# Optimization experiments

Hardware: AMD Instinct MI355X
Metric: run time of the kernel (lower is better)

Reference implementation:

```python
import jax, jax.numpy as jnp
import numpy as np

B, N, E = 2, 8192, 131072
IN_C, NF = 4, 32
F_IN = IN_C * NF          # 128, = in_channels * num_features
HID, H, OUT = 64, 8, 64   # hidden_features, nheads, out_features
NEG_SLOPE = 0.2           # GATv2Conv default negative_slope


def setup_inputs() -> dict:
    key = jax.random.key(0)
    ks = jax.random.split(key, 12)
    x = jax.random.normal(ks[0], (B, N, IN_C, NF), dtype=jnp.float32)
    edge_index = jax.random.randint(ks[1], (2, E), 0, N, dtype=jnp.int32)

    def w(k, shape, fan_in):
        return jax.random.normal(k, shape, dtype=jnp.float32) / np.sqrt(fan_in).astype(np.float32)

    # GATv2 layer 1: lin_l (source), lin_r (target), attention vector a, bias
    W1l = w(ks[2], (F_IN, H * HID), F_IN)
    W1r = w(ks[3], (F_IN, H * HID), F_IN)
    att1 = w(ks[4], (H, HID), HID)
    b1 = jnp.zeros((H * HID,), dtype=jnp.float32)
    # GATv2 layer 2: input channels = H*HID = 512
    W2l = w(ks[5], (H * HID, H * OUT), H * HID)
    W2r = w(ks[6], (H * HID, H * OUT), H * HID)
    att2 = w(ks[7], (H, OUT), OUT)
    b2 = jnp.zeros((H * OUT,), dtype=jnp.float32)
    return {"x": x, "edge_index": edge_index,
            "W1l": W1l, "W1r": W1r, "att1": att1, "b1": b1,
            "W2l": W2l, "W2r": W2r, "att2": att2, "b2": b2}


def _gatv2_layer(f, src, dst, Wl, Wr, att, b, heads, ch):
    # f: [N, F_in]; src/dst: [E'] (self-loops included)
    xl = (f @ Wl).reshape(N, heads, ch)   # source-side transform (messages)
    xr = (f @ Wr).reshape(N, heads, ch)   # target-side transform
    e = jax.nn.leaky_relu(xl[src] + xr[dst], NEG_SLOPE)     # [E', H, C]
    logits = jnp.einsum('ehc,hc->eh', e, att)               # [E', H]
    # softmax over incoming edges of each target node
    m = jax.lax.stop_gradient(jax.ops.segment_max(logits, dst, num_segments=N))
    a = jnp.exp(logits - m[dst])
    denom = jax.ops.segment_sum(a, dst, num_segments=N)     # [N, H] (>0: self-loops)
    a = a / denom[dst]
    out = jax.ops.segment_sum(xl[src] * a[:, :, None], dst, num_segments=N)
    return out.reshape(N, heads * ch) + b


def reference(x, edge_index, W1l, W1r, att1, b1, W2l, W2r, att2, b2):
    # add self-loops (PyG GATv2Conv default add_self_loops=True)
    loops = jnp.arange(N, dtype=edge_index.dtype)
    src = jnp.concatenate([edge_index[0], loops])
    dst = jnp.concatenate([edge_index[1], loops])
    feats = x.reshape(B, N, F_IN)  # view(batch, nodes, in_channels*num_features)

    def per_graph(f):
        h = _gatv2_layer(f, src, dst, W1l, W1r, att1, b1, H, HID)   # [N, 512]
        return _gatv2_layer(h, src, dst, W2l, W2r, att2, b2, H, OUT)  # [N, 512]

    h_prime = jax.vmap(per_graph)(feats)   # [B, N, H*OUT]
    return jax.nn.elu(h_prime)             # concat=True branch
```

## Files before the change

kernel.cpp:

```cpp
#include <hip/hip_runtime.h>
#include <cstdint>

#define NN 8192
#define NT 16384
#define EE 131072
#define EPAD (EE + NN)
#define SPAD (EPAD + 3 * NN)
#define FIN 128
#define CH 512
#define NH 8
#define NEG 0.2f

typedef __attribute__((ext_vector_type(8))) short short8;
typedef __attribute__((ext_vector_type(4))) unsigned short u16x4;
typedef __attribute__((ext_vector_type(4))) float f32x4;
typedef __attribute__((ext_vector_type(4))) int i32x4;

__device__ inline unsigned short bf16rne(float x) {
    unsigned u = __float_as_uint(x);
    unsigned r = (u + 0x7FFFu + ((u >> 16) & 1u)) >> 16;
    return (unsigned short)r;
}
__device__ inline float bf16tof(unsigned short h) {
    return __uint_as_float((unsigned)h << 16);
}
__device__ inline void gload16(const void* g, void* l) {
    __builtin_amdgcn_global_load_lds((const __attribute__((address_space(1))) void*)g,
                                     (__attribute__((address_space(3))) void*)l, 16, 0, 0);
}
template <int CTRL>
__device__ inline float dpp_add(float x) {
    int v = __builtin_amdgcn_update_dpp(0, __float_as_int(x), CTRL, 0xF, 0xF, true);
    return x + __int_as_float(v);
}


__global__ __launch_bounds__(256) void k_deg(const int* __restrict__ ei, int* __restrict__ deg) {
    int e = blockIdx.x * 256 + threadIdx.x;
    if (e >= EPAD) return;
    int dst = (e < EE) ? ei[EE + e] : (e - EE);
    atomicAdd(&deg[dst], 1);
}

__global__ __launch_bounds__(1024) void k_scan(const int* __restrict__ deg, int* __restrict__ rowptr) {
    __shared__ int wsum[16];
    int t = threadIdx.x;
    int lane = t & 63, wid = t >> 6;
    int loc[8];
    int s = 0;
#pragma unroll
    for (int i = 0; i < 8; i++) { loc[i] = s; s += (deg[t * 8 + i] + 3) & ~3; }
    int inc = s;
#pragma unroll
    for (int off = 1; off < 64; off <<= 1) {
        int v = __shfl_up(inc, off);
        if (lane >= off) inc += v;
    }
    if (lane == 63) wsum[wid] = inc;
    __syncthreads();
    if (wid == 0 && lane < 16) {
        int v = wsum[lane];
#pragma unroll
        for (int off = 1; off < 16; off <<= 1) {
            int u = __shfl_up(v, off);
            if (lane >= off) v += u;
        }
        wsum[lane] = v;
    }
    __syncthreads();
    int wbase = (wid == 0) ? 0 : wsum[wid - 1];
    int base = wbase + inc - s;
#pragma unroll
    for (int i = 0; i < 8; i++) rowptr[t * 8 + i] = base + loc[i];
    if (t == 1023) rowptr[NN] = wbase + inc;
}

__global__ __launch_bounds__(256) void k_scatter(const int* __restrict__ ei, const int* __restrict__ rowptr,
                                                 int* __restrict__ cursor, int* __restrict__ ssrc) {
    int e = blockIdx.x * 256 + threadIdx.x;
    if (e >= EPAD) return;
    int src = (e < EE) ? ei[e] : (e - EE);
    int dst = (e < EE) ? ei[EE + e] : (e - EE);
    int pos = rowptr[dst] + atomicAdd(&cursor[dst], 1);
    ssrc[pos] = src;
}

__global__ __launch_bounds__(256) void k_pad(const int* __restrict__ rowptr, const int* __restrict__ deg,
                                             int* __restrict__ ssrc) {
    int n = blockIdx.x * 256 + threadIdx.x;
    if (n >= NN) return;
    int e = rowptr[n] + deg[n], pe = rowptr[n + 1];
    for (int i = e; i < pe; i++) ssrc[i] = 0;
}


__global__ __launch_bounds__(256) void k_cvt_ah(const float* __restrict__ F,
                                                unsigned short* __restrict__ Ah, int n4) {
    int i = blockIdx.x * 256 + threadIdx.x;
    if (i >= n4) return;
    f32x4 v = ((const f32x4*)F)[i];
#pragma unroll
    for (int c = 0; c < 4; c++) Ah[i * 4 + c] = bf16rne(v[c]);
}

template <int K>
__global__ __launch_bounds__(256) void k_cvt_w(const float* __restrict__ Wl, const float* __restrict__ Wr,
                                               unsigned short* __restrict__ Wh) {
    int idx = blockIdx.x * 256 + threadIdx.x;
    int n = idx / K, k = idx % K;
    const float* W = (n < 512) ? Wl : Wr;
    Wh[idx] = bf16rne(W[k * 512 + (n & 511)]);
}


template <int K, int BK>
__global__ __launch_bounds__(256) void k_gemm_mfma(const unsigned short* __restrict__ Ah,
                                                   const unsigned short* __restrict__ Bh,
                                                   unsigned short* __restrict__ XLb,
                                                   float* __restrict__ XR) {
    const int NS = BK / 8;
    __shared__ unsigned short sAh[NS][128][8], sBh[NS][128][8];
    int tid = threadIdx.x;
    int l = tid & 63;
    int w = tid >> 6, wm = w >> 1, wn = w & 1;
    int m0 = blockIdx.x * 128, n0 = blockIdx.y * 128;
    int lr = l & 15, kh = l >> 4;
    f32x4 acc[4][4] = {};

    for (int k0 = 0; k0 < K; k0 += BK) {
#pragma unroll
        for (int g = 0; g < NS / 2; g++) {
            int cell = g * 256 + tid;
            int ckh = cell >> 7, cr = cell & 127;
            int ka = k0 + ckh * 8;
            gload16(Ah + (size_t)(m0 + cr) * K + ka, &sAh[ckh][cr][0]);
            gload16(Bh + (size_t)(n0 + cr) * K + ka, &sBh[ckh][cr][0]);
        }
        __syncthreads();
#pragma unroll
        for (int kk = 0; kk < BK / 32; kk++) {
            int ks = kk * 4 + kh;
            short8 fah[4], fbh[4];
#pragma unroll
            for (int i = 0; i < 4; i++) {
                fah[i] = *(const short8*)&sAh[ks][wm * 64 + i * 16 + lr][0];
                fbh[i] = *(const short8*)&sBh[ks][wn * 64 + i * 16 + lr][0];
            }
#pragma unroll
            for (int i = 0; i < 4; i++)
#pragma unroll
                for (int j = 0; j < 4; j++)
                    acc[i][j] = __builtin_amdgcn_mfma_f32_16x16x32_bf16(fah[i], fbh[j], acc[i][j], 0, 0, 0);
        }
        __syncthreads();
    }
    int colt = n0 + wn * 64;
    int cb = colt & 511;
    if (colt < 512) {
#pragma unroll
        for (int i = 0; i < 4; i++) {
            int mg = m0 + wm * 64 + i * 16 + kh * 4;
#pragma unroll
            for (int j = 0; j < 4; j++) {
                int cg = cb + j * 16 + lr;
#pragma unroll
                for (int q = 0; q < 4; q++)
                    XLb[(size_t)(mg + q) * CH + cg] = bf16rne(acc[i][j][q]);
            }
        }
    } else {
#pragma unroll
        for (int i = 0; i < 4; i++) {
            int mg = m0 + wm * 64 + i * 16 + kh * 4;
#pragma unroll
            for (int j = 0; j < 4; j++) {
                int cg = cb + j * 16 + lr;
#pragma unroll
                for (int q = 0; q < 4; q++)
                    XR[(size_t)(mg + q) * CH + cg] = acc[i][j][q];
            }
        }
    }
}


#define GATHER(CX, IV)                                                         \
  {                                                                            \
    CX[0] = *(const u16x4*)(XLg + (size_t)IV[0] * CH);                         \
    CX[1] = *(const u16x4*)(XLg + (size_t)IV[1] * CH);                         \
    CX[2] = *(const u16x4*)(XLg + (size_t)IV[2] * CH);                         \
    CX[3] = *(const u16x4*)(XLg + (size_t)IV[3] * CH);                         \
  }

#define PROCESS(CX, cb)                                                        \
  {                                                                            \
    float f[4][4];                                                             \
    _Pragma("unroll") for (int e = 0; e < 4; e++)                              \
      _Pragma("unroll") for (int r = 0; r < 4; r++)                            \
        f[e][r] = bf16tof(CX[e][r]);                                           \
    float z[4];                                                                \
    _Pragma("unroll") for (int e = 0; e < 4; e++) {                            \
      float s = 0.f;                                                           \
      _Pragma("unroll") for (int r = 0; r < 4; r++) {                          \
        float t = f[e][r] + xrv[r];                                            \
        t = fmaxf(t, NEG * t);                                                 \
        s += t * atv[r];                                                       \
      }                                                                        \
      z[e] = s;                                                                \
    }                                                                          \
    _Pragma("unroll") for (int e = 0; e < 4; e++) {                            \
      z[e] = dpp_add<0xB1>(z[e]);                                              \
      z[e] = dpp_add<0x4E>(z[e]);                                              \
      z[e] = dpp_add<0x124>(z[e]);                                             \
      z[e] = dpp_add<0x128>(z[e]);                                             \
    }                                                                          \
    _Pragma("unroll") for (int e = 1; e < 4; e++)                              \
      if ((cb) + e >= end) z[e] = -1e30f;                                      \
    float mc = fmaxf(fmaxf(z[0], z[1]), fmaxf(z[2], z[3]));                    \
    if (__ballot(mc > mh + 8.f) == 0ULL) {                                     \
      float p0 = __expf(z[0] - mh), p1 = __expf(z[1] - mh);                    \
      float p2 = __expf(z[2] - mh), p3 = __expf(z[3] - mh);                    \
      sh += (p0 + p1) + (p2 + p3);                                             \
      _Pragma("unroll") for (int r = 0; r < 4; r++)                            \
        acc[r] += p0 * f[0][r] + p1 * f[1][r] + p2 * f[2][r] + p3 * f[3][r];   \
    } else {                                                                   \
      float nm = fmaxf(mh, mc);                                                \
      float sc = __expf(mh - nm);                                              \
      float p0 = __expf(z[0] - nm), p1 = __expf(z[1] - nm);                    \
      float p2 = __expf(z[2] - nm), p3 = __expf(z[3] - nm);                    \
      sh = sh * sc + (p0 + p1) + (p2 + p3);                                    \
      mh = nm;                                                                 \
      _Pragma("unroll") for (int r = 0; r < 4; r++)                            \
        acc[r] = acc[r] * sc + p0 * f[0][r] + p1 * f[1][r] + p2 * f[2][r] +    \
                 p3 * f[3][r];                                                 \
    }                                                                          \
  }

template <int WRITE_BF16>
__global__ __launch_bounds__(256) void k_node5(const unsigned short* __restrict__ XLb,
                                               const float* __restrict__ XR,
                                               const int* __restrict__ rowptr,
                                               const int* __restrict__ deg,
                                               const int* __restrict__ ssrc,
                                               const float* __restrict__ att,
                                               const float* __restrict__ bias,
                                               float* __restrict__ OUT,
                                               unsigned short* __restrict__ OAh) {
    int w = threadIdx.x >> 6;
    int nid = blockIdx.x * 2 + (w >> 1);
    int g = w & 1;
    int l = threadIdx.x & 63;
    int node = nid & (NN - 1);
    int beg = rowptr[node], pend = rowptr[node + 1];
    int end = beg + deg[node];
    int hb = g * 256 + l * 4;

    const unsigned short* XLg = XLb + (size_t)(nid >> 13) * NN * CH + hb;
    f32x4 xrv = *(const f32x4*)(XR + (size_t)nid * CH + hb);
    f32x4 atv = *(const f32x4*)(att + hb);
    f32x4 acc = {0.f, 0.f, 0.f, 0.f};
    float mh = -1e30f, sh = 0.f;

    i32x4 iA = *(const i32x4*)(ssrc + beg);
    i32x4 iB = iA;
    u16x4 curA[4], curB[4];
    GATHER(curA, iA);
    if (beg + 4 < pend) iB = *(const i32x4*)(ssrc + beg + 4);

    int base = beg;
    while (true) {
        if (base + 4 < pend) GATHER(curB, iB);
        if (base + 8 < pend) iA = *(const i32x4*)(ssrc + base + 8);
        PROCESS(curA, base);
        base += 4;
        if (base >= pend) break;
        if (base + 4 < pend) GATHER(curA, iA);
        if (base + 8 < pend) iB = *(const i32x4*)(ssrc + base + 8);
        PROCESS(curB, base);
        base += 4;
        if (base >= pend) break;
    }

    float inv = 1.f / sh;
    f32x4 biasv = *(const f32x4*)(bias + hb);
    size_t ob = (size_t)nid * CH + hb;
    if (WRITE_BF16) {
        u16x4 hv;
#pragma unroll
        for (int r = 0; r < 4; r++) {
            float wv = acc[r] * inv + biasv[r];
            hv[r] = bf16rne(wv);
        }
        *(u16x4*)(OAh + ob) = hv;
    } else {
        f32x4 ov;
#pragma unroll
        for (int r = 0; r < 4; r++) {
            float wv = acc[r] * inv + biasv[r];
            ov[r] = (wv > 0.f) ? wv : (__expf(wv) - 1.f);
        }
        *(f32x4*)(OUT + ob) = ov;
    }
}


extern "C" void kernel_launch(void* const* d_in, const int* in_sizes, int n_in,
                              void* d_out, int out_size, void* d_ws, size_t ws_size,
                              hipStream_t stream) {
    const float* x    = (const float*)d_in[0];
    const int*   ei   = (const int*)d_in[1];
    const float* W1l  = (const float*)d_in[2];
    const float* W1r  = (const float*)d_in[3];
    const float* att1 = (const float*)d_in[4];
    const float* b1   = (const float*)d_in[5];
    const float* W2l  = (const float*)d_in[6];
    const float* W2r  = (const float*)d_in[7];
    const float* att2 = (const float*)d_in[8];
    const float* b2   = (const float*)d_in[9];
    float* out = (float*)d_out;

    char* ws = (char*)d_ws;
    int* rowptr = (int*)ws;
    int* cursor = rowptr + NN + 1;
    int* deg    = cursor + NN;
    int* ssrc   = deg + NN;
    unsigned short* XLb = (unsigned short*)(((uintptr_t)(ssrc + SPAD) + 255) & ~(uintptr_t)255);
    float* XR = (float*)(XLb + (size_t)NT * CH);
    unsigned short* A_h = (unsigned short*)(XR + (size_t)NT * CH);
    unsigned short* W1h = A_h + (size_t)NT * CH;
    unsigned short* W2h = W1h + 1024 * FIN;
    unsigned short* W2o = W2h + 1024 * CH;

    (void)W2o;
    hipMemsetAsync(cursor, 0, (size_t)2 * NN * sizeof(int), stream);
    k_deg<<<(EPAD + 255) / 256, 256, 0, stream>>>(ei, deg);
    k_scan<<<1, 1024, 0, stream>>>(deg, rowptr);
    k_scatter<<<(EPAD + 255) / 256, 256, 0, stream>>>(ei, rowptr, cursor, ssrc);
    k_pad<<<NN / 256, 256, 0, stream>>>(rowptr, deg, ssrc);
    k_cvt_w<FIN><<<1024 * FIN / 256, 256, 0, stream>>>(W1l, W1r, W1h);
    k_cvt_w<CH><<<1024 * CH / 256, 256, 0, stream>>>(W2l, W2r, W2h);

    k_cvt_ah<<<NT * FIN / 4 / 256, 256, 0, stream>>>(x, A_h, NT * FIN / 4);
    k_gemm_mfma<FIN, 64><<<dim3(NT / 128, 8), 256, 0, stream>>>(A_h, W1h, XLb, XR);
    k_node5<1><<<NT / 2, 256, 0, stream>>>(XLb, XR, rowptr, deg, ssrc, att1, b1, nullptr, A_h);
    k_gemm_mfma<CH, 64><<<dim3(NT / 128, 8), 256, 0, stream>>>(A_h, W2h, XLb, XR);
    k_node5<0><<<NT / 2, 256, 0, stream>>>(XLb, XR, rowptr, deg, ssrc, att2, b2, out, nullptr);
}
```

Measured before the change: 210.9 us.

## Double-buffer LDS tiles in MFMA GEMM with explicit vmcnt waits

Replaces the single-buffered BK=64 shared-memory loop in the bf16 MFMA GEMM with a double-buffered BK=32 pipeline. The next K-slice is prefetched into the alternate buffer while the current one is consumed, using manual s_waitcnt vmcnt and raw s_barrier with sched_barrier fences. The aim is to hide global-load latency behind MFMA work. In exchange it halves the K-step so there are more barriers per tile, and correctness depends on the hand-written vmcnt count matching the number of outstanding async loads.

```diff
diff --git a/kernel.cpp b/kernel.cpp
--- a/kernel.cpp
+++ b/kernel.cpp
@@ -113,13 +113,23 @@
 }
 
 
-template <int K, int BK>
+#define STAGE(B, k0)                                                         \
+  {                                                                          \
+    _Pragma("unroll") for (int g = 0; g < 2; g++) {                          \
+      int cell = g * 256 + tid;                                              \
+      int ckh = cell >> 7, cr = cell & 127;                                  \
+      int ka = (k0) + ckh * 8;                                               \
+      gload16(Ah + (size_t)(m0 + cr) * K + ka, &sAh[B][ckh][cr][0]);         \
+      gload16(Bh + (size_t)(n0 + cr) * K + ka, &sBh[B][ckh][cr][0]);         \
+    }                                                                        \
+  }
+
+template <int K>
 __global__ __launch_bounds__(256) void k_gemm_mfma(const unsigned short* __restrict__ Ah,
                                                    const unsigned short* __restrict__ Bh,
                                                    unsigned short* __restrict__ XLb,
                                                    float* __restrict__ XR) {
-    const int NS = BK / 8;
-    __shared__ unsigned short sAh[NS][128][8], sBh[NS][128][8];
+    __shared__ unsigned short sAh[2][4][128][8], sBh[2][4][128][8];
     int tid = threadIdx.x;
     int l = tid & 63;
     int w = tid >> 6, wm = w >> 1, wn = w & 1;
@@ -127,32 +137,32 @@
     int lr = l & 15, kh = l >> 4;
     f32x4 acc[4][4] = {};
 
-    for (int k0 = 0; k0 < K; k0 += BK) {
-#pragma unroll
-        for (int g = 0; g < NS / 2; g++) {
-            int cell = g * 256 + tid;
-            int ckh = cell >> 7, cr = cell & 127;
-            int ka = k0 + ckh * 8;
-            gload16(Ah + (size_t)(m0 + cr) * K + ka, &sAh[ckh][cr][0]);
-            gload16(Bh + (size_t)(n0 + cr) * K + ka, &sBh[ckh][cr][0]);
-        }
-        __syncthreads();
-#pragma unroll
-        for (int kk = 0; kk < BK / 32; kk++) {
-            int ks = kk * 4 + kh;
-            short8 fah[4], fbh[4];
-#pragma unroll
-            for (int i = 0; i < 4; i++) {
-                fah[i] = *(const short8*)&sAh[ks][wm * 64 + i * 16 + lr][0];
-                fbh[i] = *(const short8*)&sBh[ks][wn * 64 + i * 16 + lr][0];
-            }
-#pragma unroll
-            for (int i = 0; i < 4; i++)
-#pragma unroll
-                for (int j = 0; j < 4; j++)
-                    acc[i][j] = __builtin_amdgcn_mfma_f32_16x16x32_bf16(fah[i], fbh[j], acc[i][j], 0, 0, 0);
-        }
-        __syncthreads();
+    STAGE(0, 0);
+    int buf = 0;
+    for (int k0 = 0; k0 < K; k0 += 32) {
+        if (k0 + 32 < K) {
+            STAGE(buf ^ 1, k0 + 32);
+            asm volatile("s_waitcnt vmcnt(4)" ::: "memory");
+        } else {
+            asm volatile("s_waitcnt vmcnt(0)" ::: "memory");
+        }
+        __builtin_amdgcn_sched_barrier(0);
+        __builtin_amdgcn_s_barrier();
+        __builtin_amdgcn_sched_barrier(0);
+        short8 fah[4], fbh[4];
+#pragma unroll
+        for (int i = 0; i < 4; i++) {
+            fah[i] = *(const short8*)&sAh[buf][kh][wm * 64 + i * 16 + lr][0];
+            fbh[i] = *(const short8*)&sBh[buf][kh][wn * 64 + i * 16 + lr][0];
+        }
+#pragma unroll
+        for (int i = 0; i < 4; i++)
+#pragma unroll
+            for (int j = 0; j < 4; j++)
+                acc[i][j] = __builtin_amdgcn_mfma_f32_16x16x32_bf16(fah[i], fbh[j], acc[i][j], 0, 0, 0);
+        __builtin_amdgcn_sched_barrier(0);
+        __builtin_amdgcn_s_barrier();
+        buf ^= 1;
     }
     int colt = n0 + wn * 64;
     int cb = colt & 511;
@@ -329,9 +339,7 @@
     unsigned short* A_h = (unsigned short*)(XR + (size_t)NT * CH);
     unsigned short* W1h = A_h + (size_t)NT * CH;
     unsigned short* W2h = W1h + 1024 * FIN;
-    unsigned short* W2o = W2h + 1024 * CH;
-
-    (void)W2o;
+
     hipMemsetAsync(cursor, 0, (size_t)2 * NN * sizeof(int), stream);
     k_deg<<<(EPAD + 255) / 256, 256, 0, stream>>>(ei, deg);
     k_scan<<<1, 1024, 0, stream>>>(deg, rowptr);
@@ -341,8 +349,8 @@
     k_cvt_w<CH><<<1024 * CH / 256, 256, 0, stream>>>(W2l, W2r, W2h);
 
     k_cvt_ah<<<NT * FIN / 4 / 256, 256, 0, stream>>>(x, A_h, NT * FIN / 4);
-    k_gemm_mfma<FIN, 64><<<dim3(NT / 128, 8), 256, 0, stream>>>(A_h, W1h, XLb, XR);
+    k_gemm_mfma<FIN><<<dim3(NT / 128, 8), 256, 0, stream>>>(A_h, W1h, XLb, XR);
     k_node5<1><<<NT / 2, 256, 0, stream>>>(XLb, XR, rowptr, deg, ssrc, att1, b1, nullptr, A_h);
-    k_gemm_mfma<CH, 64><<<dim3(NT / 128, 8), 256, 0, stream>>>(A_h, W2h, XLb, XR);
+    k_gemm_mfma<CH><<<dim3(NT / 128, 8), 256, 0, stream>>>(A_h, W2h, XLb, XR);
     k_node5<0><<<NT / 2, 256, 0, stream>>>(XLb, XR, rowptr, deg, ssrc, att2, b2, out, nullptr);
 }
```

After: 210.9 us. Within noise of the previous version (-0.0%).
